# Kernel optimization log

Measured on AMD Instinct MI355X. Metric: run time of the kernel, lower is better.

## Reference

```python
import jax, jax.numpy as jnp
import numpy as np

B, S, DIM = 2, 2048, 2048
H, QLR, KVLR = 16, 1536, 512
D_NOPE, D_ROPE, D_QK, D_V = 128, 64, 192, 128
EPS = 1e-6


def rms_norm(x, w, eps=EPS):
    return x * jax.lax.rsqrt(jnp.mean(jnp.square(x), axis=-1, keepdims=True) + eps) * w


def rope(x, theta):
    # x: [b, s, n, d], theta: [s, d//2] rotation angles
    xr = x.reshape(*x.shape[:-1], -1, 2)
    x0, x1 = xr[..., 0], xr[..., 1]
    cos = jnp.cos(theta)[None, :, None, :]
    sin = jnp.sin(theta)[None, :, None, :]
    out = jnp.stack([x0 * cos - x1 * sin, x0 * sin + x1 * cos], axis=-1)
    return out.reshape(x.shape).astype(x.dtype)


def setup_inputs() -> dict:
    key = jax.random.key(0)
    ks = jax.random.split(key, 6)
    x = jax.random.normal(ks[0], (B, S, DIM), jnp.float32)
    # standard RoPE angles theta[s, i] = s / 10000^(2i/d_rope)
    pos = jnp.arange(S, dtype=jnp.float32)
    inv = 1.0 / (10000.0 ** (jnp.arange(0, D_ROPE, 2, dtype=jnp.float32) / D_ROPE))
    freqs = pos[:, None] * inv[None, :]  # [S, D_ROPE//2]
    sc = lambda k, shp: jax.random.normal(k, shp, jnp.float32) * (1.0 / np.sqrt(shp[0]))
    return {
        'x': x,
        'freqs': freqs,
        'start_pos': 0,
        'wq_a': sc(ks[1], (DIM, QLR)),
        'q_norm_w': jnp.ones((QLR,), jnp.float32),
        'wq_b': sc(ks[2], (QLR, H * D_QK)),
        'wkv_a': sc(ks[3], (DIM, KVLR + D_ROPE)),
        'kv_norm_w': jnp.ones((KVLR,), jnp.float32),
        'wkv_b': sc(ks[4], (KVLR, H * (D_NOPE + D_V))),
        'wo': sc(ks[5], (H * D_V, DIM)),
    }


def reference(x, freqs, start_pos, wq_a, q_norm_w, wq_b, wkv_a, kv_norm_w, wkv_b, wo):
    bsz, seqlen, _ = x.shape
    scale = D_QK ** -0.5
    # low-rank Q: down-proj -> RMSNorm -> up-proj
    q = rms_norm(x @ wq_a, q_norm_w) @ wq_b
    q = q.reshape(bsz, seqlen, H, D_QK)
    q_nope, q_pe = q[..., :D_NOPE], q[..., D_NOPE:]
    q_pe = rope(q_pe, freqs)
    # low-rank KV: joint down-proj, split latent / rope part
    kv = x @ wkv_a
    c_kv, k_pe = kv[..., :KVLR], kv[..., KVLR:]
    k_pe = rope(k_pe[:, :, None, :], freqs)[:, :, 0, :]  # [b, t, r]
    # weight absorption: fold wkv_b's k_nope block into q
    wkv_b_mat = wkv_b.T.reshape(H, D_NOPE + D_V, KVLR)  # [h, d_nope+d_v, c]
    q_abs = jnp.einsum('bshd,hdc->bshc', q_nope, wkv_b_mat[:, :D_NOPE])
    kv_cache = rms_norm(c_kv, kv_norm_w)  # [b, t, c] compressed KV cache
    scores = (jnp.einsum('bshc,btc->bsht', q_abs, kv_cache)
              + jnp.einsum('bshr,btr->bsht', q_pe, k_pe)) * scale
    causal = jnp.tril(jnp.ones((seqlen, seqlen), bool))  # prefill, start_pos=0
    scores = jnp.where(causal[None, :, None, :], scores, -1e9)
    attn = jax.nn.softmax(scores.astype(jnp.float32), axis=-1).astype(x.dtype)
    # attend in latent space, then up-project with the v block of wkv_b
    o = jnp.einsum('bsht,btc->bshc', attn, kv_cache)
    o = jnp.einsum('bshc,hdc->bshd', o, wkv_b_mat[:, D_NOPE:])
    return o.reshape(bsz, seqlen, H * D_V) @ wo
```

## Files before the change

kernel.cpp:

```cpp
#include <hip/hip_runtime.h>

typedef __bf16 bf16x8 __attribute__((ext_vector_type(8)));
typedef float floatx4 __attribute__((ext_vector_type(4)));

#define MFMA(a, b, c) __builtin_amdgcn_mfma_f32_16x16x32_bf16((a), (b), (c), 0, 0, 0)

__device__ __forceinline__ float bf2f(ushort u) {
    union { unsigned int i; float f; } v; v.i = ((unsigned int)u) << 16; return v.f;
}
__device__ __forceinline__ ushort f2bf(float f) {
    union { float f; unsigned int i; } v; v.f = f;
    unsigned int r = v.i + 0x7fffu + ((v.i >> 16) & 1u);
    return (ushort)(r >> 16);
}
__device__ __forceinline__ bf16x8 ldb8(const ushort* p) { return *(const bf16x8*)p; }

__global__ __launch_bounds__(256) void transpose_f32_bf16(
    const float* __restrict__ in, ushort* __restrict__ out, int R, int C) {
    __shared__ ushort tile[32][33];
    const int c0 = blockIdx.x * 32, r0 = blockIdx.y * 32;
    const int tx = threadIdx.x, ty = threadIdx.y;
    #pragma unroll
    for (int i = 0; i < 32; i += 8) {
        int r = r0 + ty + i, c = c0 + tx;
        if (r < R && c < C) tile[ty + i][tx] = f2bf(in[(long)r * C + c]);
    }
    __syncthreads();
    #pragma unroll
    for (int i = 0; i < 32; i += 8) {
        int r = c0 + ty + i, c = r0 + tx;
        if (r < C && c < R) out[(long)r * R + c] = tile[tx][ty + i];
    }
}

__global__ __launch_bounds__(256) void cvt_f32_bf16(
    const float* __restrict__ in, ushort* __restrict__ out, long n) {
    const long i = ((long)blockIdx.x * 256 + threadIdx.x) * 4;
    if (i >= n) return;
    float4 v = *(const float4*)(in + i);
    ushort4 o;
    o.x = f2bf(v.x); o.y = f2bf(v.y); o.z = f2bf(v.z); o.w = f2bf(v.w);
    *(ushort4*)(out + i) = o;
}

__global__ __launch_bounds__(256, 2) void gemm_bt(
    const ushort* __restrict__ A, const ushort* __restrict__ Bt,
    void* __restrict__ C, int K, int lda, int ldb, int ldc,
    long aZ, long bZ, long cZ, int c_f32) {
    __shared__ __align__(16) ushort As[64][72];
    __shared__ __align__(16) ushort Bs[64][72];
    const int z = blockIdx.z;
    const ushort* Ab = A + (long)z * aZ;
    const ushort* Bb = Bt + (long)z * bZ;
    const long m0 = (long)blockIdx.y * 64;
    const long n0 = (long)blockIdx.x * 64;
    const int tid = threadIdx.x;
    const int lane = tid & 63, w = tid >> 6;
    const int wm = (w >> 1) * 32, wn = (w & 1) * 32;
    const int lrow = lane & 15, quad = lane >> 4;

    floatx4 acc[2][2] = {};

    const int r0_ = tid >> 3, c0_ = (tid & 7) * 8;
    const int r1_ = r0_ + 32, c1_ = c0_;

    for (int k0 = 0; k0 < K; k0 += 64) {
        uint4 a0 = *(const uint4*)(Ab + (m0 + r0_) * lda + k0 + c0_);
        uint4 a1 = *(const uint4*)(Ab + (m0 + r1_) * lda + k0 + c1_);
        uint4 b0 = *(const uint4*)(Bb + (n0 + r0_) * ldb + k0 + c0_);
        uint4 b1 = *(const uint4*)(Bb + (n0 + r1_) * ldb + k0 + c1_);
        __syncthreads();
        *(uint4*)&As[r0_][c0_] = a0;
        *(uint4*)&As[r1_][c1_] = a1;
        *(uint4*)&Bs[r0_][c0_] = b0;
        *(uint4*)&Bs[r1_][c1_] = b1;
        __syncthreads();
        #pragma unroll
        for (int kk = 0; kk < 64; kk += 32) {
            bf16x8 af0 = ldb8(&As[wm + lrow][kk + quad * 8]);
            bf16x8 af1 = ldb8(&As[wm + 16 + lrow][kk + quad * 8]);
            bf16x8 bf0 = ldb8(&Bs[wn + lrow][kk + quad * 8]);
            bf16x8 bf1 = ldb8(&Bs[wn + 16 + lrow][kk + quad * 8]);
            acc[0][0] = MFMA(af0, bf0, acc[0][0]);
            acc[0][1] = MFMA(af0, bf1, acc[0][1]);
            acc[1][0] = MFMA(af1, bf0, acc[1][0]);
            acc[1][1] = MFMA(af1, bf1, acc[1][1]);
        }
    }
    if (c_f32) {
        float* Cb = (float*)C + (long)z * cZ;
        #pragma unroll
        for (int mt = 0; mt < 2; ++mt)
            #pragma unroll
            for (int nt = 0; nt < 2; ++nt)
                #pragma unroll
                for (int r = 0; r < 4; ++r)
                    Cb[(m0 + wm + mt * 16 + quad * 4 + r) * ldc + n0 + wn + nt * 16 + lrow] = acc[mt][nt][r];
    } else {
        ushort* Cb = (ushort*)C + (long)z * cZ;
        #pragma unroll
        for (int mt = 0; mt < 2; ++mt)
            #pragma unroll
            for (int nt = 0; nt < 2; ++nt)
                #pragma unroll
                for (int r = 0; r < 4; ++r)
                    Cb[(m0 + wm + mt * 16 + quad * 4 + r) * ldc + n0 + wn + nt * 16 + lrow] = f2bf(acc[mt][nt][r]);
    }
}

__global__ __launch_bounds__(256, 2) void gemm_bt128(
    const ushort* __restrict__ A, const ushort* __restrict__ Bt,
    void* __restrict__ C, int K, int lda, int ldb, int ldc,
    long aZ, long bZ, long cZ, int c_f32) {
    __shared__ __align__(16) ushort As[128 * 64];
    __shared__ __align__(16) ushort Bs[128 * 64];
    const int z = blockIdx.z;
    const ushort* Ab = A + (long)z * aZ;
    const ushort* Bb = Bt + (long)z * bZ;
    const long m0 = (long)blockIdx.y * 128;
    const long n0 = (long)blockIdx.x * 128;
    const int tid = threadIdx.x;
    const int lane = tid & 63, w = tid >> 6;
    const int wm = (w >> 1) * 64, wn = (w & 1) * 64;
    const int lrow = lane & 15, quad = lane >> 4;

    floatx4 acc[4][4] = {};

    for (int k0 = 0; k0 < K; k0 += 64) {
        __syncthreads();
        #pragma unroll
        for (int t = 0; t < 4; ++t) {
            const int c = t * 256 + tid;
            const int r = c >> 3, kc = (c & 7) * 8;
            __builtin_amdgcn_global_load_lds(
                (const __attribute__((address_space(1))) unsigned int*)(Ab + (m0 + r) * lda + k0 + kc),
                (__attribute__((address_space(3))) unsigned int*)(As + (long)c * 8), 16, 0, 0);
            __builtin_amdgcn_global_load_lds(
                (const __attribute__((address_space(1))) unsigned int*)(Bb + (n0 + r) * ldb + k0 + kc),
                (__attribute__((address_space(3))) unsigned int*)(Bs + (long)c * 8), 16, 0, 0);
        }
        __syncthreads();
        #pragma unroll
        for (int kk = 0; kk < 64; kk += 32) {
            bf16x8 af[4], bv[4];
            #pragma unroll
            for (int i = 0; i < 4; ++i) {
                af[i] = ldb8(&As[(wm + i * 16 + lrow) * 64 + kk + quad * 8]);
                bv[i] = ldb8(&Bs[(wn + i * 16 + lrow) * 64 + kk + quad * 8]);
            }
            #pragma unroll
            for (int i = 0; i < 4; ++i)
                #pragma unroll
                for (int j = 0; j < 4; ++j)
                    acc[i][j] = MFMA(af[i], bv[j], acc[i][j]);
        }
    }
    if (c_f32) {
        float* Cb = (float*)C + (long)z * cZ;
        #pragma unroll
        for (int mt = 0; mt < 4; ++mt)
            #pragma unroll
            for (int nt = 0; nt < 4; ++nt)
                #pragma unroll
                for (int r = 0; r < 4; ++r)
                    Cb[(m0 + wm + mt * 16 + quad * 4 + r) * ldc + n0 + wn + nt * 16 + lrow] = acc[mt][nt][r];
    } else {
        ushort* Cb = (ushort*)C + (long)z * cZ;
        #pragma unroll
        for (int mt = 0; mt < 4; ++mt)
            #pragma unroll
            for (int nt = 0; nt < 4; ++nt)
                #pragma unroll
                for (int r = 0; r < 4; ++r)
                    Cb[(m0 + wm + mt * 16 + quad * 4 + r) * ldc + n0 + wn + nt * 16 + lrow] = f2bf(acc[mt][nt][r]);
    }
}

__global__ __launch_bounds__(256) void rms1536(
    const ushort* in, const float* __restrict__ w, ushort* out) {
    const int row = blockIdx.x, t = threadIdx.x;
    const ushort* ip = in + (long)row * 1536;
    float v[6]; float ss = 0.f;
    #pragma unroll
    for (int i = 0; i < 6; ++i) { v[i] = bf2f(ip[i * 256 + t]); ss += v[i] * v[i]; }
    __shared__ float red[256];
    red[t] = ss; __syncthreads();
    for (int st = 128; st > 0; st >>= 1) { if (t < st) red[t] += red[t + st]; __syncthreads(); }
    const float sc = rsqrtf(red[0] * (1.f / 1536.f) + 1e-6f);
    ushort* op = out + (long)row * 1536;
    #pragma unroll
    for (int i = 0; i < 6; ++i) op[i * 256 + t] = f2bf(v[i] * sc * w[i * 256 + t]);
}

__global__ __launch_bounds__(256) void qrope(
    const ushort* __restrict__ q, const float* __restrict__ freqs,
    ushort* __restrict__ qpe) {
    const int tok = blockIdx.x;
    const int s = tok & 2047;
    const int t = threadIdx.x;
    #pragma unroll
    for (int p = 0; p < 2; ++p) {
        const int idx = p * 256 + t;
        const int h = idx >> 5, i = idx & 31;
        const long base = (long)tok * 3072 + h * 192 + 128 + 2 * i;
        float x0 = bf2f(q[base]), x1 = bf2f(q[base + 1]);
        float th = freqs[s * 32 + i];
        float sn = sinf(th), cs = cosf(th);
        const long ob = (long)tok * 1024 + h * 64 + 2 * i;
        qpe[ob]     = f2bf(x0 * cs - x1 * sn);
        qpe[ob + 1] = f2bf(x0 * sn + x1 * cs);
    }
}

__global__ __launch_bounds__(256) void kvprep(
    const ushort* __restrict__ kv, const float* __restrict__ w,
    const float* __restrict__ freqs, ushort* __restrict__ kvc,
    ushort* __restrict__ kpe) {
    const int tok = blockIdx.x;
    const int s = tok & 2047;
    const int t = threadIdx.x;
    const float v0 = bf2f(kv[(long)tok * 576 + t]);
    const float v1 = bf2f(kv[(long)tok * 576 + 256 + t]);
    __shared__ float red[256];
    red[t] = v0 * v0 + v1 * v1; __syncthreads();
    for (int st = 128; st > 0; st >>= 1) { if (t < st) red[t] += red[t + st]; __syncthreads(); }
    const float sc = rsqrtf(red[0] * (1.f / 512.f) + 1e-6f);
    kvc[(long)tok * 512 + t] = f2bf(v0 * sc * w[t]);
    kvc[(long)tok * 512 + 256 + t] = f2bf(v1 * sc * w[256 + t]);
    if (t < 32) {
        float x0 = bf2f(kv[(long)tok * 576 + 512 + 2 * t]);
        float x1 = bf2f(kv[(long)tok * 576 + 512 + 2 * t + 1]);
        float th = freqs[s * 32 + t];
        float sn = sinf(th), cs = cosf(th);
        kpe[(long)tok * 64 + 2 * t]     = f2bf(x0 * cs - x1 * sn);
        kpe[(long)tok * 64 + 2 * t + 1] = f2bf(x0 * sn + x1 * cs);
    }
}

__global__ __launch_bounds__(256, 2) void mha_attn(
    const ushort* __restrict__ q,
    const ushort* __restrict__ qpe,
    const ushort* __restrict__ kn,
    const ushort* __restrict__ kpe,
    const ushort* __restrict__ vT,
    ushort* __restrict__ o2) {
    __shared__ __align__(16) ushort Ks[128][200];
    __shared__ __align__(16) ushort P[64][136];
    const int qx = blockIdx.x, h = blockIdx.y, b = blockIdx.z;
    const int tid = threadIdx.x, lane = tid & 63, w = tid >> 6;
    const int lrow = lane & 15, quad = lane >> 4;
    const long bb = (long)b * 2048;
    const float scale = 0.07216878364870323f;
    const int rn = tid >> 4, cn = (tid & 15) * 8;
    const int rr = tid >> 3, cr = (tid & 7) * 8;

    for (int half = 0; half < 2; ++half) {
        const int qt = half ? (31 - qx) : qx;
        const int qrow = qt * 64;
        const long tokb = bb + qrow;

        bf16x8 qa[6];
        {
            const ushort* qp_ = q + (tokb + w * 16 + lrow) * 3072 + h * 192 + quad * 8;
            #pragma unroll
            for (int ks = 0; ks < 4; ++ks) qa[ks] = ldb8(qp_ + ks * 32);
            const ushort* qq = qpe + (tokb + w * 16 + lrow) * 1024 + h * 64 + quad * 8;
            qa[4] = ldb8(qq); qa[5] = ldb8(qq + 32);
        }

        floatx4 oacc[4][2] = {};
        float m_i[4], l_i[4];
        #pragma unroll
        for (int r = 0; r < 4; ++r) { m_i[r] = -1e30f; l_i[r] = 0.f; }

        const int niter = qt / 2 + 1;
        for (int t = 0; t < niter; ++t) {
            const int kv0 = t * 128;
            {
                const ushort* src = kn + (bb + kv0 + rn) * 2048 + h * 128 + cn;
                #pragma unroll
                for (int j = 0; j < 8; ++j) {
                    uint4 v = *(const uint4*)(src + (long)j * 16 * 2048);
                    *(uint4*)&Ks[j * 16 + rn][cn] = v;
                }
                const ushort* srp = kpe + (bb + kv0 + rr) * 64 + cr;
                #pragma unroll
                for (int j = 0; j < 4; ++j) {
                    uint4 v = *(const uint4*)(srp + (long)j * 32 * 64);
                    *(uint4*)&Ks[j * 32 + rr][128 + cr] = v;
                }
            }
            __syncthreads();

            floatx4 sacc[8] = {};
            __builtin_amdgcn_s_setprio(1);
            #pragma unroll
            for (int f = 0; f < 8; ++f)
                #pragma unroll
                for (int ks = 0; ks < 6; ++ks)
                    sacc[f] = MFMA(qa[ks], ldb8(&Ks[f * 16 + lrow][ks * 32 + quad * 8]), sacc[f]);
            __builtin_amdgcn_s_setprio(0);

            bf16x8 vf[2][4];
            {
                const ushort* vb = vT + ((long)(b * 16 + h)) * 262144 + (long)(w * 32 + lrow) * 2048 + kv0 + quad * 8;
                #pragma unroll
                for (int nf = 0; nf < 2; ++nf)
                    #pragma unroll
                    for (int kk = 0; kk < 4; ++kk)
                        vf[nf][kk] = ldb8(vb + (long)nf * 16 * 2048 + kk * 32);
            }

            #pragma unroll
            for (int r = 0; r < 4; ++r) {
                const int rloc = w * 16 + quad * 4 + r;
                const int row_s = qrow + rloc;
                float pv[8];
                float smax = -1e30f;
                #pragma unroll
                for (int f = 0; f < 8; ++f) {
                    pv[f] = sacc[f][r] * scale;
                    if (kv0 + f * 16 + lrow > row_s) pv[f] = -1e30f;
                    smax = fmaxf(smax, pv[f]);
                }
                #pragma unroll
                for (int off = 1; off < 16; off <<= 1)
                    smax = fmaxf(smax, __shfl_xor(smax, off));
                const float mnew = fmaxf(m_i[r], smax);
                const float alpha = __expf(m_i[r] - mnew);
                float ps = 0.f;
                #pragma unroll
                for (int f = 0; f < 8; ++f) {
                    float p = __expf(pv[f] - mnew);
                    P[rloc][f * 16 + lrow] = f2bf(p);
                    ps += p;
                }
                #pragma unroll
                for (int off = 1; off < 16; off <<= 1)
                    ps += __shfl_xor(ps, off);
                l_i[r] = l_i[r] * alpha + ps;
                m_i[r] = mnew;
                if (lrow == 0) *(float*)&P[rloc][128] = alpha;
            }
            __syncthreads();

            __builtin_amdgcn_s_setprio(1);
            #pragma unroll
            for (int mf = 0; mf < 4; ++mf) {
                float al[4];
                #pragma unroll
                for (int r = 0; r < 4; ++r) al[r] = *(const float*)&P[mf * 16 + quad * 4 + r][128];
                const int need = (al[0] != 1.f) | (al[1] != 1.f) | (al[2] != 1.f) | (al[3] != 1.f);
                if (__any(need)) {
                    #pragma unroll
                    for (int nf = 0; nf < 2; ++nf)
                        #pragma unroll
                        for (int r = 0; r < 4; ++r) oacc[mf][nf][r] *= al[r];
                }
                #pragma unroll
                for (int kk = 0; kk < 4; ++kk) {
                    bf16x8 pf = ldb8(&P[mf * 16 + lrow][kk * 32 + quad * 8]);
                    oacc[mf][0] = MFMA(pf, vf[0][kk], oacc[mf][0]);
                    oacc[mf][1] = MFMA(pf, vf[1][kk], oacc[mf][1]);
                }
            }
            __builtin_amdgcn_s_setprio(0);
        }

        #pragma unroll
        for (int r = 0; r < 4; ++r)
            if (lrow == 0) *(float*)&P[w * 16 + quad * 4 + r][132] = l_i[r];
        __syncthreads();
        #pragma unroll
        for (int mf = 0; mf < 4; ++mf) {
            float li[4];
            #pragma unroll
            for (int r = 0; r < 4; ++r) li[r] = *(const float*)&P[mf * 16 + quad * 4 + r][132];
            #pragma unroll
            for (int nf = 0; nf < 2; ++nf)
                #pragma unroll
                for (int r = 0; r < 4; ++r) {
                    long tok = tokb + mf * 16 + quad * 4 + r;
                    o2[tok * 2048 + h * 128 + w * 32 + nf * 16 + lrow] = f2bf(oacc[mf][nf][r] / li[r]);
                }
        }
        __syncthreads();
    }
}

extern "C" void kernel_launch(void* const* d_in, const int* in_sizes, int n_in,
                              void* d_out, int out_size, void* d_ws, size_t ws_size,
                              hipStream_t stream) {
    const float* x      = (const float*)d_in[0];
    const float* freqs  = (const float*)d_in[1];
    const float* wq_a   = (const float*)d_in[3];
    const float* qnw    = (const float*)d_in[4];
    const float* wq_b   = (const float*)d_in[5];
    const float* wkv_a  = (const float*)d_in[6];
    const float* kvnw   = (const float*)d_in[7];
    const float* wkv_b  = (const float*)d_in[8];
    const float* wo     = (const float*)d_in[9];
    float* out = (float*)d_out;
    (void)ws_size; (void)in_sizes; (void)n_in; (void)out_size;

    char* ws = (char*)d_ws;
    ushort* q_lat  = (ushort*)(ws + 0);
    ushort* o2     = (ushort*)(ws + 0);
    ushort* xb     = (ushort*)(ws + 16777216);
    ushort* knope  = (ushort*)(ws + 16777216);
    ushort* q      = (ushort*)(ws + 33554432);
    ushort* qpe    = (ushort*)(ws + 58720256);
    ushort* kv     = (ushort*)(ws + 67108864);
    ushort* kvc    = (ushort*)(ws + 71827456);
    ushort* kpe    = (ushort*)(ws + 76021760);
    ushort* vT     = (ushort*)(ws + 76546048);
    ushort* wq_aT  = (ushort*)(ws + 93323264);
    ushort* wq_bT  = (ushort*)(ws + 99614720);
    ushort* wkv_aT = (ushort*)(ws + 109051904);
    ushort* wkv_bT = (ushort*)(ws + 111411200);
    ushort* woT    = (ushort*)(ws + 115605504);

    dim3 tb(32, 8);
    transpose_f32_bf16<<<dim3(48, 64), tb, 0, stream>>>(wq_a, wq_aT, 2048, 1536);
    transpose_f32_bf16<<<dim3(96, 48), tb, 0, stream>>>(wq_b, wq_bT, 1536, 3072);
    transpose_f32_bf16<<<dim3(18, 64), tb, 0, stream>>>(wkv_a, wkv_aT, 2048, 576);
    transpose_f32_bf16<<<dim3(128, 16), tb, 0, stream>>>(wkv_b, wkv_bT, 512, 4096);
    transpose_f32_bf16<<<dim3(64, 64), tb, 0, stream>>>(wo, woT, 2048, 2048);
    cvt_f32_bf16<<<8192, 256, 0, stream>>>(x, xb, 8388608L);

    gemm_bt128<<<dim3(12, 32, 1), 256, 0, stream>>>(xb, wq_aT, q_lat, 2048, 2048, 2048, 1536, 0, 0, 0, 0);
    rms1536<<<4096, 256, 0, stream>>>(q_lat, qnw, q_lat);
    gemm_bt128<<<dim3(24, 32, 1), 256, 0, stream>>>(q_lat, wq_bT, q, 1536, 1536, 1536, 3072, 0, 0, 0, 0);
    qrope<<<4096, 256, 0, stream>>>(q, freqs, qpe);
    gemm_bt<<<dim3(9, 64, 1), 256, 0, stream>>>(xb, wkv_aT, kv, 2048, 2048, 2048, 576, 0, 0, 0, 0);
    kvprep<<<4096, 256, 0, stream>>>(kv, kvnw, freqs, kvc, kpe);

    gemm_bt128<<<dim3(1, 16, 16), 256, 0, stream>>>(kvc, wkv_bT, knope,
        512, 512, 512, 2048, 0, 131072, 128, 0);
    gemm_bt128<<<dim3(1, 16, 16), 256, 0, stream>>>(kvc + 1048576, wkv_bT, knope + 4194304,
        512, 512, 512, 2048, 0, 131072, 128, 0);
    gemm_bt128<<<dim3(16, 1, 16), 256, 0, stream>>>(wkv_bT + 65536, kvc, vT,
        512, 512, 512, 2048, 131072, 0, 262144, 0);
    gemm_bt128<<<dim3(16, 1, 16), 256, 0, stream>>>(wkv_bT + 65536, kvc + 1048576, vT + 4194304,
        512, 512, 512, 2048, 131072, 0, 262144, 0);

    mha_attn<<<dim3(16, 16, 2), 256, 0, stream>>>(q, qpe, knope, kpe, vT, o2);

    gemm_bt128<<<dim3(16, 32, 1), 256, 0, stream>>>(o2, woT, out, 2048, 2048, 2048, 2048, 0, 0, 0, 1);
}
```

Measured before the change: 509.9 us.

## Merge Q and KV down-projections, precompute RoPE table, remap attention blocks

Concatenates wq_a and wkv_a into a single transposed weight so one 2176-wide GEMM produces both the Q latent and the KV latent, and drops the 64-tile GEMM. Adds a cos/sin table kernel so the RoPE kernels load precomputed values instead of calling sinf/cosf. Replaces the shared-memory tree reductions in the RMS kernels with wave shuffles. In attention, the score scale is folded with log2(e) so exp2 can be used, and block IDs are remapped so blocks sharing a head and batch land on the same XCD for L2 reuse. The trade-off is a different workspace layout and an extra small kernel launch.

```diff
diff --git a/kernel.cpp b/kernel.cpp
--- a/kernel.cpp
+++ b/kernel.cpp
@@ -43,69 +43,11 @@
     *(ushort4*)(out + i) = o;
 }
 
-__global__ __launch_bounds__(256, 2) void gemm_bt(
-    const ushort* __restrict__ A, const ushort* __restrict__ Bt,
-    void* __restrict__ C, int K, int lda, int ldb, int ldc,
-    long aZ, long bZ, long cZ, int c_f32) {
-    __shared__ __align__(16) ushort As[64][72];
-    __shared__ __align__(16) ushort Bs[64][72];
-    const int z = blockIdx.z;
-    const ushort* Ab = A + (long)z * aZ;
-    const ushort* Bb = Bt + (long)z * bZ;
-    const long m0 = (long)blockIdx.y * 64;
-    const long n0 = (long)blockIdx.x * 64;
-    const int tid = threadIdx.x;
-    const int lane = tid & 63, w = tid >> 6;
-    const int wm = (w >> 1) * 32, wn = (w & 1) * 32;
-    const int lrow = lane & 15, quad = lane >> 4;
-
-    floatx4 acc[2][2] = {};
-
-    const int r0_ = tid >> 3, c0_ = (tid & 7) * 8;
-    const int r1_ = r0_ + 32, c1_ = c0_;
-
-    for (int k0 = 0; k0 < K; k0 += 64) {
-        uint4 a0 = *(const uint4*)(Ab + (m0 + r0_) * lda + k0 + c0_);
-        uint4 a1 = *(const uint4*)(Ab + (m0 + r1_) * lda + k0 + c1_);
-        uint4 b0 = *(const uint4*)(Bb + (n0 + r0_) * ldb + k0 + c0_);
-        uint4 b1 = *(const uint4*)(Bb + (n0 + r1_) * ldb + k0 + c1_);
-        __syncthreads();
-        *(uint4*)&As[r0_][c0_] = a0;
-        *(uint4*)&As[r1_][c1_] = a1;
-        *(uint4*)&Bs[r0_][c0_] = b0;
-        *(uint4*)&Bs[r1_][c1_] = b1;
-        __syncthreads();
-        #pragma unroll
-        for (int kk = 0; kk < 64; kk += 32) {
-            bf16x8 af0 = ldb8(&As[wm + lrow][kk + quad * 8]);
-            bf16x8 af1 = ldb8(&As[wm + 16 + lrow][kk + quad * 8]);
-            bf16x8 bf0 = ldb8(&Bs[wn + lrow][kk + quad * 8]);
-            bf16x8 bf1 = ldb8(&Bs[wn + 16 + lrow][kk + quad * 8]);
-            acc[0][0] = MFMA(af0, bf0, acc[0][0]);
-            acc[0][1] = MFMA(af0, bf1, acc[0][1]);
-            acc[1][0] = MFMA(af1, bf0, acc[1][0]);
-            acc[1][1] = MFMA(af1, bf1, acc[1][1]);
-        }
-    }
-    if (c_f32) {
-        float* Cb = (float*)C + (long)z * cZ;
-        #pragma unroll
-        for (int mt = 0; mt < 2; ++mt)
-            #pragma unroll
-            for (int nt = 0; nt < 2; ++nt)
-                #pragma unroll
-                for (int r = 0; r < 4; ++r)
-                    Cb[(m0 + wm + mt * 16 + quad * 4 + r) * ldc + n0 + wn + nt * 16 + lrow] = acc[mt][nt][r];
-    } else {
-        ushort* Cb = (ushort*)C + (long)z * cZ;
-        #pragma unroll
-        for (int mt = 0; mt < 2; ++mt)
-            #pragma unroll
-            for (int nt = 0; nt < 2; ++nt)
-                #pragma unroll
-                for (int r = 0; r < 4; ++r)
-                    Cb[(m0 + wm + mt * 16 + quad * 4 + r) * ldc + n0 + wn + nt * 16 + lrow] = f2bf(acc[mt][nt][r]);
-    }
+__global__ __launch_bounds__(256) void trigtab(
+    const float* __restrict__ freqs, float2* __restrict__ trig) {
+    const int idx = blockIdx.x * 256 + threadIdx.x;
+    float th = freqs[idx];
+    trig[idx] = make_float2(cosf(th), sinf(th));
 }
 
 __global__ __launch_bounds__(256, 2) void gemm_bt128(
@@ -177,23 +119,26 @@
 }
 
 __global__ __launch_bounds__(256) void rms1536(
-    const ushort* in, const float* __restrict__ w, ushort* out) {
+    ushort* qk, const float* __restrict__ w) {
     const int row = blockIdx.x, t = threadIdx.x;
-    const ushort* ip = in + (long)row * 1536;
+    const int lane = t & 63, wv = t >> 6;
+    ushort* ip = qk + (long)row * 2176;
     float v[6]; float ss = 0.f;
     #pragma unroll
     for (int i = 0; i < 6; ++i) { v[i] = bf2f(ip[i * 256 + t]); ss += v[i] * v[i]; }
-    __shared__ float red[256];
-    red[t] = ss; __syncthreads();
-    for (int st = 128; st > 0; st >>= 1) { if (t < st) red[t] += red[t + st]; __syncthreads(); }
-    const float sc = rsqrtf(red[0] * (1.f / 1536.f) + 1e-6f);
-    ushort* op = out + (long)row * 1536;
-    #pragma unroll
-    for (int i = 0; i < 6; ++i) op[i * 256 + t] = f2bf(v[i] * sc * w[i * 256 + t]);
+    #pragma unroll
+    for (int off = 32; off > 0; off >>= 1) ss += __shfl_xor(ss, off);
+    __shared__ float red[4];
+    if (lane == 0) red[wv] = ss;
+    __syncthreads();
+    const float tot = red[0] + red[1] + red[2] + red[3];
+    const float sc = rsqrtf(tot * (1.f / 1536.f) + 1e-6f);
+    #pragma unroll
+    for (int i = 0; i < 6; ++i) ip[i * 256 + t] = f2bf(v[i] * sc * w[i * 256 + t]);
 }
 
 __global__ __launch_bounds__(256) void qrope(
-    const ushort* __restrict__ q, const float* __restrict__ freqs,
+    const ushort* __restrict__ q, const float2* __restrict__ trig,
     ushort* __restrict__ qpe) {
     const int tok = blockIdx.x;
     const int s = tok & 2047;
@@ -204,36 +149,40 @@
         const int h = idx >> 5, i = idx & 31;
         const long base = (long)tok * 3072 + h * 192 + 128 + 2 * i;
         float x0 = bf2f(q[base]), x1 = bf2f(q[base + 1]);
-        float th = freqs[s * 32 + i];
-        float sn = sinf(th), cs = cosf(th);
+        float2 cs = trig[s * 32 + i];
         const long ob = (long)tok * 1024 + h * 64 + 2 * i;
-        qpe[ob]     = f2bf(x0 * cs - x1 * sn);
-        qpe[ob + 1] = f2bf(x0 * sn + x1 * cs);
+        qpe[ob]     = f2bf(x0 * cs.x - x1 * cs.y);
+        qpe[ob + 1] = f2bf(x0 * cs.y + x1 * cs.x);
     }
 }
 
 __global__ __launch_bounds__(256) void kvprep(
-    const ushort* __restrict__ kv, const float* __restrict__ w,
-    const float* __restrict__ freqs, ushort* __restrict__ kvc,
+    const ushort* __restrict__ qk, const float* __restrict__ w,
+    const float2* __restrict__ trig, ushort* __restrict__ kvc,
     ushort* __restrict__ kpe) {
     const int tok = blockIdx.x;
     const int s = tok & 2047;
     const int t = threadIdx.x;
-    const float v0 = bf2f(kv[(long)tok * 576 + t]);
-    const float v1 = bf2f(kv[(long)tok * 576 + 256 + t]);
-    __shared__ float red[256];
-    red[t] = v0 * v0 + v1 * v1; __syncthreads();
-    for (int st = 128; st > 0; st >>= 1) { if (t < st) red[t] += red[t + st]; __syncthreads(); }
-    const float sc = rsqrtf(red[0] * (1.f / 512.f) + 1e-6f);
+    const int lane = t & 63, wv = t >> 6;
+    const ushort* in2 = qk + (long)tok * 2176 + 1536;
+    const float v0 = bf2f(in2[t]);
+    const float v1 = bf2f(in2[256 + t]);
+    float ss = v0 * v0 + v1 * v1;
+    #pragma unroll
+    for (int off = 32; off > 0; off >>= 1) ss += __shfl_xor(ss, off);
+    __shared__ float red[4];
+    if (lane == 0) red[wv] = ss;
+    __syncthreads();
+    const float tot = red[0] + red[1] + red[2] + red[3];
+    const float sc = rsqrtf(tot * (1.f / 512.f) + 1e-6f);
     kvc[(long)tok * 512 + t] = f2bf(v0 * sc * w[t]);
     kvc[(long)tok * 512 + 256 + t] = f2bf(v1 * sc * w[256 + t]);
     if (t < 32) {
-        float x0 = bf2f(kv[(long)tok * 576 + 512 + 2 * t]);
-        float x1 = bf2f(kv[(long)tok * 576 + 512 + 2 * t + 1]);
-        float th = freqs[s * 32 + t];
-        float sn = sinf(th), cs = cosf(th);
-        kpe[(long)tok * 64 + 2 * t]     = f2bf(x0 * cs - x1 * sn);
-        kpe[(long)tok * 64 + 2 * t + 1] = f2bf(x0 * sn + x1 * cs);
+        float x0 = bf2f(in2[512 + 2 * t]);
+        float x1 = bf2f(in2[512 + 2 * t + 1]);
+        float2 cs = trig[s * 32 + t];
+        kpe[(long)tok * 64 + 2 * t]     = f2bf(x0 * cs.x - x1 * cs.y);
+        kpe[(long)tok * 64 + 2 * t + 1] = f2bf(x0 * cs.y + x1 * cs.x);
     }
 }
 
@@ -246,11 +195,14 @@
     ushort* __restrict__ o2) {
     __shared__ __align__(16) ushort Ks[128][200];
     __shared__ __align__(16) ushort P[64][136];
-    const int qx = blockIdx.x, h = blockIdx.y, b = blockIdx.z;
+    const int fid = blockIdx.x + (blockIdx.y << 4) + (blockIdx.z << 8);
+    const int xcd = fid & 7, j = fid >> 3;
+    const int g = xcd * 4 + (j >> 4);
+    const int qx = j & 15, h = g & 15, b = g >> 4;
     const int tid = threadIdx.x, lane = tid & 63, w = tid >> 6;
     const int lrow = lane & 15, quad = lane >> 4;
     const long bb = (long)b * 2048;
-    const float scale = 0.07216878364870323f;
+    const float scale = 0.07216878364870323f * 1.4426950408889634f;
     const int rn = tid >> 4, cn = (tid & 15) * 8;
     const int rr = tid >> 3, cr = (tid & 7) * 8;
 
@@ -279,15 +231,15 @@
             {
                 const ushort* src = kn + (bb + kv0 + rn) * 2048 + h * 128 + cn;
                 #pragma unroll
-                for (int j = 0; j < 8; ++j) {
-                    uint4 v = *(const uint4*)(src + (long)j * 16 * 2048);
-                    *(uint4*)&Ks[j * 16 + rn][cn] = v;
+                for (int j2 = 0; j2 < 8; ++j2) {
+                    uint4 v = *(const uint4*)(src + (long)j2 * 16 * 2048);
+                    *(uint4*)&Ks[j2 * 16 + rn][cn] = v;
                 }
                 const ushort* srp = kpe + (bb + kv0 + rr) * 64 + cr;
                 #pragma unroll
-                for (int j = 0; j < 4; ++j) {
-                    uint4 v = *(const uint4*)(srp + (long)j * 32 * 64);
-                    *(uint4*)&Ks[j * 32 + rr][128 + cr] = v;
+                for (int j2 = 0; j2 < 4; ++j2) {
+                    uint4 v = *(const uint4*)(srp + (long)j2 * 32 * 64);
+                    *(uint4*)&Ks[j2 * 32 + rr][128 + cr] = v;
                 }
             }
             __syncthreads();
@@ -327,11 +279,11 @@
                 for (int off = 1; off < 16; off <<= 1)
                     smax = fmaxf(smax, __shfl_xor(smax, off));
                 const float mnew = fmaxf(m_i[r], smax);
-                const float alpha = __expf(m_i[r] - mnew);
+                const float alpha = __builtin_amdgcn_exp2f(m_i[r] - mnew);
                 float ps = 0.f;
                 #pragma unroll
                 for (int f = 0; f < 8; ++f) {
-                    float p = __expf(pv[f] - mnew);
+                    float p = __builtin_amdgcn_exp2f(pv[f] - mnew);
                     P[rloc][f * 16 + lrow] = f2bf(p);
                     ps += p;
                 }
@@ -404,36 +356,35 @@
     (void)ws_size; (void)in_sizes; (void)n_in; (void)out_size;
 
     char* ws = (char*)d_ws;
-    ushort* q_lat  = (ushort*)(ws + 0);
-    ushort* o2     = (ushort*)(ws + 0);
-    ushort* xb     = (ushort*)(ws + 16777216);
-    ushort* knope  = (ushort*)(ws + 16777216);
-    ushort* q      = (ushort*)(ws + 33554432);
-    ushort* qpe    = (ushort*)(ws + 58720256);
-    ushort* kv     = (ushort*)(ws + 67108864);
-    ushort* kvc    = (ushort*)(ws + 71827456);
-    ushort* kpe    = (ushort*)(ws + 76021760);
-    ushort* vT     = (ushort*)(ws + 76546048);
-    ushort* wq_aT  = (ushort*)(ws + 93323264);
-    ushort* wq_bT  = (ushort*)(ws + 99614720);
-    ushort* wkv_aT = (ushort*)(ws + 109051904);
-    ushort* wkv_bT = (ushort*)(ws + 111411200);
-    ushort* woT    = (ushort*)(ws + 115605504);
+    ushort* qk_comb = (ushort*)(ws + 0);
+    ushort* o2      = (ushort*)(ws + 0);
+    ushort* xb      = (ushort*)(ws + 17825792);
+    ushort* knope   = (ushort*)(ws + 17825792);
+    ushort* q       = (ushort*)(ws + 34603008);
+    ushort* qpe     = (ushort*)(ws + 59768832);
+    ushort* kvc     = (ushort*)(ws + 68157440);
+    ushort* kpe     = (ushort*)(ws + 72351744);
+    ushort* vT      = (ushort*)(ws + 72876032);
+    ushort* wcombT  = (ushort*)(ws + 89653248);
+    ushort* wq_bT   = (ushort*)(ws + 98566144);
+    ushort* wkv_bT  = (ushort*)(ws + 108003328);
+    ushort* woT     = (ushort*)(ws + 112197632);
+    float2* trig    = (float2*)(ws + 120586240);
 
     dim3 tb(32, 8);
-    transpose_f32_bf16<<<dim3(48, 64), tb, 0, stream>>>(wq_a, wq_aT, 2048, 1536);
+    trigtab<<<256, 256, 0, stream>>>(freqs, trig);
+    transpose_f32_bf16<<<dim3(48, 64), tb, 0, stream>>>(wq_a, wcombT, 2048, 1536);
+    transpose_f32_bf16<<<dim3(18, 64), tb, 0, stream>>>(wkv_a, wcombT + 1536L * 2048, 2048, 576);
     transpose_f32_bf16<<<dim3(96, 48), tb, 0, stream>>>(wq_b, wq_bT, 1536, 3072);
-    transpose_f32_bf16<<<dim3(18, 64), tb, 0, stream>>>(wkv_a, wkv_aT, 2048, 576);
     transpose_f32_bf16<<<dim3(128, 16), tb, 0, stream>>>(wkv_b, wkv_bT, 512, 4096);
     transpose_f32_bf16<<<dim3(64, 64), tb, 0, stream>>>(wo, woT, 2048, 2048);
     cvt_f32_bf16<<<8192, 256, 0, stream>>>(x, xb, 8388608L);
 
-    gemm_bt128<<<dim3(12, 32, 1), 256, 0, stream>>>(xb, wq_aT, q_lat, 2048, 2048, 2048, 1536, 0, 0, 0, 0);
-    rms1536<<<4096, 256, 0, stream>>>(q_lat, qnw, q_lat);
-    gemm_bt128<<<dim3(24, 32, 1), 256, 0, stream>>>(q_lat, wq_bT, q, 1536, 1536, 1536, 3072, 0, 0, 0, 0);
-    qrope<<<4096, 256, 0, stream>>>(q, freqs, qpe);
-    gemm_bt<<<dim3(9, 64, 1), 256, 0, stream>>>(xb, wkv_aT, kv, 2048, 2048, 2048, 576, 0, 0, 0, 0);
-    kvprep<<<4096, 256, 0, stream>>>(kv, kvnw, freqs, kvc, kpe);
+    gemm_bt128<<<dim3(17, 32, 1), 256, 0, stream>>>(xb, wcombT, qk_comb, 2048, 2048, 2048, 2176, 0, 0, 0, 0);
+    rms1536<<<4096, 256, 0, stream>>>(qk_comb, qnw);
+    gemm_bt128<<<dim3(24, 32, 1), 256, 0, stream>>>(qk_comb, wq_bT, q, 1536, 2176, 1536, 3072, 0, 0, 0, 0);
+    qrope<<<4096, 256, 0, stream>>>(q, trig, qpe);
+    kvprep<<<4096, 256, 0, stream>>>(qk_comb, kvnw, trig, kvc, kpe);
 
     gemm_bt128<<<dim3(1, 16, 16), 256, 0, stream>>>(kvc, wkv_bT, knope,
         512, 512, 512, 2048, 0, 131072, 128, 0);
```

Result: faster. 488.1 us (-4.3%).
